# Kernel tuning notes

Measured on AMD Instinct MI355X. Metric: run time of the kernel, lower is better.

The kernel has to match this reference:

```python
import jax, jax.numpy as jnp
import numpy as np

K = 256           # number of selected features (init kwarg k)
NUM_SAMPLES = 8   # init kwarg num_samples
BATCH = 256
NUM_FEATURES = 20000


def setup_inputs() -> dict:
    key = jax.random.key(0)
    logits = jax.random.normal(key, (BATCH, NUM_FEATURES, 1), dtype=jnp.float32)
    return {"logits": logits, "tau": 1, "training": 0}


def reference(logits, tau, training):
    # Eval branch of SubsetLayer.forward (training=False).
    # logits: [B, N, 1]
    B, N, _ = logits.shape
    scores = logits[..., 0]                       # [B, N]
    _, idx = jax.lax.top_k(scores, K)             # idx: [B, K]
    # k-hot mask built directly by scatter (equivalent to one_hot(...).sum(1))
    khot = jnp.zeros((B, N), dtype=jnp.float32)
    khot = khot.at[jnp.arange(B)[:, None], idx].set(1.0)  # [B, N]
    # unsqueeze(0).unsqueeze(-1).expand(num_samples, -1, -1, -1)
    out = jnp.broadcast_to(khot[None, :, :, None], (NUM_SAMPLES, B, N, 1))
    return out
```

## Files before the change

kernel.cpp:

```cpp
#include <hip/hip_runtime.h>

#define BATCH   256
#define NFEAT   20000
#define NVEC    (NFEAT / 4)
#define KSEL    256
#define NSAMP   8
#define CAP     2048

typedef unsigned long long u64;
typedef float __attribute__((ext_vector_type(4))) f32x4;

#define BAR() do { asm volatile("s_waitcnt lgkmcnt(0)" ::: "memory"); \
                   __builtin_amdgcn_s_barrier();                      \
                   asm volatile("" ::: "memory"); } while (0)

__device__ __forceinline__ unsigned fmap(float f) {
    unsigned u = __float_as_uint(f);
    return (u & 0x80000000u) ? ~u : (u | 0x80000000u);
}

__device__ __forceinline__ void select_bin_wave0(const unsigned* hist, int nbins, int w,
                                                 int* s_d, int* s_w, int lane) {
    for (int base = nbins - 1; base >= 0; base -= 64) {
        int bin = base - lane;
        unsigned c = (bin >= 0) ? hist[bin] : 0u;
        unsigned p = c;
#pragma unroll
        for (int off = 1; off < 64; off <<= 1) {
            unsigned t = __shfl_up(p, off);
            if (lane >= off) p += t;
        }
        unsigned long long m = __ballot(p >= (unsigned)w);
        if (m) {
            int l = __ffsll(m) - 1;
            if (lane == l) { *s_d = bin; *s_w = w - (int)(p - c); }
            return;
        }
        w -= (int)__shfl(p, 63);
    }
    if (lane == 0) { *s_d = 0; *s_w = 1; }
}

__device__ __forceinline__ void pick64(const unsigned* arr, int w, int lane,
                                       int* s_idx, int* s_w) {
    unsigned c = arr[63 - lane];
    unsigned p = c;
#pragma unroll
    for (int off = 1; off < 64; off <<= 1) {
        unsigned t = __shfl_up(p, off);
        if (lane >= off) p += t;
    }
    unsigned long long m = __ballot(p >= (unsigned)w);
    if (m) {
        int l = __ffsll(m) - 1;
        if (lane == l) { *s_idx = 63 - l; *s_w = w - (int)(p - c); }
    } else if (lane == 0) { *s_idx = 0; *s_w = 1; }
}

__global__ __launch_bounds__(1024) void topk_fused(const float* __restrict__ logits,
                                                   float* __restrict__ out) {
    const int b = blockIdx.x, tid = threadIdx.x;
    const int lane = tid & 63, wave = tid >> 6;
    const float4* __restrict__ row4 = (const float4*)(logits + (size_t)b * NFEAT);
    const size_t BN = (size_t)BATCH * NFEAT;
    float* const outb = out + (size_t)b * NFEAT;
    const f32x4 z4 = {0.0f, 0.0f, 0.0f, 0.0f};

#define ZSTORE(J)                                                              \
    do {                                                                       \
        const int i4_ = tid + (J) * 1024;                                      \
        if (i4_ < NVEC) {                                                      \
            _Pragma("unroll")                                                  \
            for (int s_ = 0; s_ < NSAMP; ++s_)                                 \
                *reinterpret_cast<f32x4*>(outb + (size_t)s_ * BN + 4 * i4_) = z4; \
        }                                                                      \
    } while (0)

    __shared__ unsigned hist[4096];
    __shared__ u64 cand[CAP];
    __shared__ unsigned csum[64];
    __shared__ int s_d, s_w;
    __shared__ unsigned s_cnt;
    __shared__ u64 s_thr;
    __shared__ int s_run, s_cut, s_wc[16];

    float4 v[5];
#pragma unroll
    for (int j = 0; j < 5; ++j) {
        const int i4 = tid + j * 1024;
        v[j] = row4[(i4 < NVEC) ? i4 : (NVEC - 1)];
    }
    ZSTORE(0);
    ZSTORE(1);
#pragma unroll
    for (int j = 0; j < 4; ++j) hist[tid + j * 1024] = 0;
    BAR();

    unsigned kk[5][4];
#pragma unroll
    for (int j = 0; j < 5; ++j) {
        kk[j][0] = fmap(v[j].x); kk[j][1] = fmap(v[j].y);
        kk[j][2] = fmap(v[j].z); kk[j][3] = fmap(v[j].w);
    }
#pragma unroll
    for (int j = 0; j < 4; ++j) {
#pragma unroll
        for (int e = 0; e < 4; ++e) atomicAdd(&hist[kk[j][e] >> 20], 1u);
    }
    if (tid + 4096 < NVEC) {
#pragma unroll
        for (int e = 0; e < 4; ++e) atomicAdd(&hist[kk[4][e] >> 20], 1u);
    }
    ZSTORE(2);
    BAR();

    unsigned keypref; int w;
    {
#pragma unroll
        for (int j = 0; j < 4; ++j) {
            const int c = wave * 4 + j;
            unsigned x = hist[c * 64 + lane];
#pragma unroll
            for (int off = 32; off; off >>= 1) x += __shfl_down(x, off);
            if (lane == 0) csum[c] = x;
        }
        BAR();
        if (wave == 0) pick64(csum, KSEL, lane, &s_d, &s_w);
        BAR();
        const int chunk = s_d; const int w0 = s_w;
        if (wave == 0) pick64(&hist[chunk * 64], w0, lane, &s_d, &s_w);
        if (tid == 0) s_cnt = 0;
        BAR();
        keypref = (unsigned)(chunk * 64 + s_d);
        w = s_w;
    }
    int shift = 20;
    ZSTORE(3);

    unsigned C;
    for (;;) {
#pragma unroll
        for (int j = 0; j < 5; ++j) {
            const int i4 = tid + j * 1024;
            if (i4 < NVEC) {
#pragma unroll
                for (int e = 0; e < 4; ++e) {
                    const unsigned k = kk[j][e];
                    if ((k >> shift) == keypref) {
                        unsigned p = atomicAdd(&s_cnt, 1u);
                        if (p < CAP) cand[p] = ((u64)k << 32) | (unsigned)~(4 * i4 + e);
                    }
                }
            }
        }
        BAR();
        C = s_cnt;
        if (C <= CAP || shift == 0) break;

        const int nb = (shift >= 12) ? 12 : shift;
        const int nsh = shift - nb;
        for (int i = tid; i < (1 << nb); i += 1024) hist[i] = 0;
        BAR();
#pragma unroll
        for (int j = 0; j < 5; ++j) {
            const int i4 = tid + j * 1024;
            if (i4 < NVEC) {
#pragma unroll
                for (int e = 0; e < 4; ++e) {
                    const unsigned k = kk[j][e];
                    if ((k >> shift) == keypref)
                        atomicAdd(&hist[(k >> nsh) & ((1u << nb) - 1u)], 1u);
                }
            }
        }
        BAR();
        if (wave == 0) select_bin_wave0(hist, 1 << nb, w, &s_d, &s_w, lane);
        if (tid == 0) s_cnt = 0;
        BAR();
        keypref = (keypref << nb) | (unsigned)s_d;
        w = s_w;
        shift = nsh;
    }
    ZSTORE(4);

    if (C <= CAP) {
        for (int i = tid; i < (int)C; i += 1024) {
            const u64 ci = cand[i];
            int cgt = 0;
            for (int j = 0; j < (int)C; ++j) cgt += (cand[j] > ci) ? 1 : 0;
            if (cgt == w - 1) s_thr = ci;
        }
        BAR();
    } else {
        if (tid == 0) { s_run = 0; s_cut = 0; }
        BAR();
#pragma unroll 1
        for (int j = 0; j < 5; ++j) {
            const int i4 = tid + j * 1024;
            bool eq[4];
            int cnt4 = 0;
#pragma unroll
            for (int e = 0; e < 4; ++e) {
                eq[e] = (i4 < NVEC) && (kk[j][e] == keypref);
                cnt4 += eq[e] ? 1 : 0;
            }
            unsigned p = (unsigned)cnt4;
#pragma unroll
            for (int off = 1; off < 64; off <<= 1) {
                unsigned t = __shfl_up(p, off);
                if (lane >= off) p += t;
            }
            const unsigned excl = p - (unsigned)cnt4;
            if (lane == 63) s_wc[wave] = (int)p;
            BAR();
            int off0 = s_run + (int)excl;
            for (int x = 0; x < wave; ++x) off0 += s_wc[x];
#pragma unroll
            for (int e = 0; e < 4; ++e) {
                if (eq[e]) { if (off0 == w - 1) s_cut = 4 * i4 + e; ++off0; }
            }
            BAR();
            if (tid == 0) { int t = 0; for (int x = 0; x < 16; ++x) t += s_wc[x]; s_run += t; }
            BAR();
            if (s_run >= w) break;
        }
        if (tid == 0) s_thr = ((u64)keypref << 32) | (unsigned)~s_cut;
        BAR();
    }

    const u64 thr = s_thr;
    const unsigned thr_k = (unsigned)(thr >> 32);
    const unsigned thr_l = (unsigned)thr;
    asm volatile("s_waitcnt vmcnt(0)" ::: "memory");
#pragma unroll
    for (int j = 0; j < 5; ++j) {
        const int i4 = tid + j * 1024;
        if (i4 < NVEC) {
            const int n = 4 * i4;
#pragma unroll
            for (int e = 0; e < 4; ++e) {
                const unsigned k = kk[j][e];
                const bool sel = (k > thr_k) || (k == thr_k && (unsigned)~(n + e) >= thr_l);
                if (sel) {
#pragma unroll
                    for (int s = 0; s < NSAMP; ++s)
                        outb[(size_t)s * BN + n + e] = 1.0f;
                }
            }
        }
    }
#undef ZSTORE
}

extern "C" void kernel_launch(void* const* d_in, const int* in_sizes, int n_in,
                              void* d_out, int out_size, void* d_ws, size_t ws_size,
                              hipStream_t stream) {
    const float* logits = (const float*)d_in[0];
    float* out = (float*)d_out;
    (void)d_ws; (void)ws_size;

    topk_fused<<<BATCH, 1024, 0, stream>>>(logits, out);
}
```

Before: 34.64 us.

## Replace quadratic candidate rank search with iterative radix select over candidates

The final threshold selection among up to CAP candidates previously had each thread compare its candidate against all others, which costs quadratic work in shared memory. It now runs repeated 12-bit radix histogram passes over the 64-bit candidate keys, narrowing the prefix until one candidate remains or all bits are resolved. This cuts work when the candidate count is large, but adds several barriers and histogram clears per pass, which may cost more when the candidate count is small.

```diff
diff --git a/kernel.cpp b/kernel.cpp
--- a/kernel.cpp
+++ b/kernel.cpp
@@ -118,11 +118,11 @@
     {
 #pragma unroll
         for (int j = 0; j < 4; ++j) {
-            const int c = wave * 4 + j;
-            unsigned x = hist[c * 64 + lane];
+            const int cc = wave * 4 + j;
+            unsigned x = hist[cc * 64 + lane];
 #pragma unroll
             for (int off = 32; off; off >>= 1) x += __shfl_down(x, off);
-            if (lane == 0) csum[c] = x;
+            if (lane == 0) csum[cc] = x;
         }
         BAR();
         if (wave == 0) pick64(csum, KSEL, lane, &s_d, &s_w);
@@ -184,13 +184,60 @@
     ZSTORE(4);
 
     if (C <= CAP) {
-        for (int i = tid; i < (int)C; i += 1024) {
-            const u64 ci = cand[i];
-            int cgt = 0;
-            for (int j = 0; j < (int)C; ++j) cgt += (cand[j] > ci) ? 1 : 0;
-            if (cgt == w - 1) s_thr = ci;
-        }
-        BAR();
+        u64 pfx = keypref;
+        int pshift = 32 + shift;
+        bool done = false;
+        while (!done) {
+            const int nb = (pshift >= 12) ? 12 : pshift;
+            const int nsh = pshift - nb;
+            const int nbins = 1 << nb;
+            for (int i = tid; i < nbins; i += 1024) hist[i] = 0;
+            BAR();
+            for (int i = tid; i < (int)C; i += 1024) {
+                const u64 cd = cand[i];
+                if ((cd >> pshift) == pfx)
+                    atomicAdd(&hist[(unsigned)(cd >> nsh) & (unsigned)(nbins - 1)], 1u);
+            }
+            BAR();
+            unsigned d;
+            if (nb == 12) {
+#pragma unroll
+                for (int j = 0; j < 4; ++j) {
+                    const int cc = wave * 4 + j;
+                    unsigned x = hist[cc * 64 + lane];
+#pragma unroll
+                    for (int off = 32; off; off >>= 1) x += __shfl_down(x, off);
+                    if (lane == 0) csum[cc] = x;
+                }
+                BAR();
+                if (wave == 0) pick64(csum, w, lane, &s_d, &s_w);
+                BAR();
+                const int chunk = s_d; const int w0 = s_w;
+                if (wave == 0) pick64(&hist[chunk * 64], w0, lane, &s_d, &s_w);
+                BAR();
+                d = (unsigned)(chunk * 64 + s_d);
+            } else {
+                if (wave == 0) select_bin_wave0(hist, nbins, w, &s_d, &s_w, lane);
+                BAR();
+                d = (unsigned)s_d;
+            }
+            w = s_w;
+            const unsigned cnt = hist[d];
+            pfx = (pfx << nb) | d;
+            pshift = nsh;
+            if (cnt == 1u || pshift == 0) {
+                if (cnt == 1u && pshift > 0) {
+                    for (int i = tid; i < (int)C; i += 1024) {
+                        const u64 cd = cand[i];
+                        if ((cd >> pshift) == pfx) s_thr = cd;
+                    }
+                } else if (tid == 0) {
+                    s_thr = pfx;
+                }
+                done = true;
+            }
+            BAR();
+        }
     } else {
         if (tid == 0) { s_run = 0; s_cut = 0; }
         BAR();
```

New measurement: 36.47 us. 5.3% more time.
